# Optimization experiments

Hardware: AMD Instinct MI355X
Metric: run time of the kernel (lower is better)

Reference implementation:

```python
import jax, jax.numpy as jnp
import numpy as np

B, T, C, H = 4, 2048, 1024, 16
D = C // H  # head_dim = 64


def setup_inputs() -> dict:
    key = jax.random.key(0)
    ks = jax.random.split(key, 5)
    scale = 0.02
    return {
        "x": jax.random.normal(ks[0], (B, T, C), dtype=jnp.float32),
        "w_qkv": jax.random.normal(ks[1], (C, 3 * C), dtype=jnp.float32) * scale,
        "b_qkv": jnp.zeros((3 * C,), dtype=jnp.float32),
        "w_out": jax.random.normal(ks[2], (C, C), dtype=jnp.float32) * scale,
        "b_out": jnp.zeros((C,), dtype=jnp.float32),
    }


def reference(x, w_qkv, b_qkv, w_out, b_out):
    Bx, Tx, Cx = x.shape
    qkv = x @ w_qkv + b_qkv  # [B,T,3C]
    q, k, v = jnp.split(qkv, 3, axis=-1)
    # [B,T,C] -> [B,H,T,D]
    def heads(t):
        return t.reshape(Bx, Tx, H, D).transpose(0, 2, 1, 3)
    q, k, v = heads(q), heads(k), heads(v)
    scores = jnp.einsum("bhtd,bhsd->bhts", q, k) / jnp.sqrt(jnp.float32(D))
    causal = jnp.tril(jnp.ones((Tx, Tx), dtype=bool))
    scores = jnp.where(causal[None, None], scores, -jnp.inf)
    attn = jax.nn.softmax(scores, axis=-1)
    y = jnp.einsum("bhts,bhsd->bhtd", attn, v)  # [B,H,T,D]
    y = y.transpose(0, 2, 1, 3).reshape(Bx, Tx, Cx)
    return y @ w_out + b_out
```

## Files before the change

kernel.cpp:

```cpp
#include <hip/hip_runtime.h>
#include <hip/hip_bf16.h>
#include <math.h>

typedef __bf16 bf16;
typedef __bf16 bf16x8 __attribute__((ext_vector_type(8)));
typedef __bf16 bf16x4 __attribute__((ext_vector_type(4)));
typedef __bf16 bf16x2 __attribute__((ext_vector_type(2)));
typedef float  f32x4  __attribute__((ext_vector_type(4)));

__device__ __forceinline__ void gld_lds16(const bf16* g, bf16* l) {
    void* gv = (void*)g;
    __builtin_amdgcn_global_load_lds(
        (__attribute__((address_space(1))) void*)gv,
        (__attribute__((address_space(3))) void*)l, 16, 0, 0);
}

__global__ void k_cvt_bf16(const float* __restrict__ in, bf16* __restrict__ out, int n4) {
    int i = blockIdx.x * blockDim.x + threadIdx.x;
    if (i < n4) {
        float4 v = ((const float4*)in)[i];
        bf16x4 o;
        o[0] = (bf16)v.x; o[1] = (bf16)v.y; o[2] = (bf16)v.z; o[3] = (bf16)v.w;
        ((bf16x4*)out)[i] = o;
    }
}

__global__ void k_transpose_cvt(const float* __restrict__ in, bf16* __restrict__ out,
                                int R, int C) {
    __shared__ float tile[64][68];
    int c0 = blockIdx.x * 64, r0 = blockIdx.y * 64;
    int tid = threadIdx.x;
#pragma unroll
    for (int i = 0; i < 4; ++i) {
        int chunk = tid + i * 256;
        int r = chunk >> 4, c4 = (chunk & 15) * 4;
        float4 v = *(const float4*)(in + (size_t)(r0 + r) * C + c0 + c4);
        tile[r][c4 + 0] = v.x; tile[r][c4 + 1] = v.y;
        tile[r][c4 + 2] = v.z; tile[r][c4 + 3] = v.w;
    }
    __syncthreads();
#pragma unroll
    for (int i = 0; i < 2; ++i) {
        int chunk = tid + i * 256;
        int c = chunk >> 3, k8 = (chunk & 7) * 8;
        bf16x8 v;
#pragma unroll
        for (int j = 0; j < 8; ++j) v[j] = (bf16)tile[k8 + j][c];
        *(bf16x8*)(out + (size_t)(c0 + c) * R + r0 + k8) = v;
    }
}

__global__ void k_transpose_v(const bf16* __restrict__ qkv, bf16* __restrict__ vt) {
    __shared__ bf16 tile[64][72];
    int bh = blockIdx.y, b = bh >> 4, h = bh & 15;
    int t0 = blockIdx.x * 64;
    int tid = threadIdx.x;
    const bf16* src = qkv + (size_t)(b * 2048 + t0) * 3072 + 2048 + h * 64;
#pragma unroll
    for (int i = 0; i < 2; ++i) {
        int chunk = tid + i * 256;
        int t = chunk >> 3, d8 = (chunk & 7) * 8;
        bf16x8 v = *(const bf16x8*)(src + (size_t)t * 3072 + d8);
#pragma unroll
        for (int j = 0; j < 8; ++j) tile[t][d8 + j] = v[j];
    }
    __syncthreads();
#pragma unroll
    for (int i = 0; i < 2; ++i) {
        int chunk = tid + i * 256;
        int d = chunk >> 3, t8 = (chunk & 7) * 8;
        bf16x8 v;
#pragma unroll
        for (int j = 0; j < 8; ++j) v[j] = tile[t8 + j][d];
        *(bf16x8*)(vt + ((size_t)bh * 64 + d) * 2048 + t0 + t8) = v;
    }
}

template <bool OUT_BF16>
__global__ __launch_bounds__(256, 2) void k_gemm(
    const bf16* __restrict__ A, const bf16* __restrict__ Bt,
    const float* __restrict__ bias, void* __restrict__ Cout,
    int M, int N, int K) {
    __shared__ __align__(16) bf16 lA[2][4096];
    __shared__ __align__(16) bf16 lB[2][4096];
    int tid = threadIdx.x;
    int wid = tid >> 6, lane = tid & 63;
    int quad = lane >> 4, l16 = lane & 15;
    int bm = blockIdx.y * 128, bn = blockIdx.x * 128;
    int wm = (wid >> 1) * 64, wn = (wid & 1) * 64;

    f32x4 zero = {0.f, 0.f, 0.f, 0.f};
    f32x4 acc[4][4];
#pragma unroll
    for (int i = 0; i < 4; ++i)
#pragma unroll
        for (int j = 0; j < 4; ++j) acc[i][j] = zero;

    for (int k0 = 0; k0 < K; k0 += 64) {
        __syncthreads();
#pragma unroll
        for (int i = 0; i < 4; ++i) {
            int j = (wid * 4 + i) * 64 + lane;
            int kf = j >> 9, row = (j & 511) >> 2, c8 = (j & 3) * 8;
            gld_lds16(A  + (size_t)(bm + row) * K + k0 + kf * 32 + c8, &lA[0][0] + (wid * 4 + i) * 512);
            gld_lds16(Bt + (size_t)(bn + row) * K + k0 + kf * 32 + c8, &lB[0][0] + (wid * 4 + i) * 512);
        }
        __syncthreads();
#pragma unroll
        for (int kk = 0; kk < 2; ++kk) {
            bf16x8 af[4], bg[4];
#pragma unroll
            for (int i = 0; i < 4; ++i) {
                af[i] = *(const bf16x8*)(&lA[kk][(wm + i * 16 + l16) * 32 + quad * 8]);
                bg[i] = *(const bf16x8*)(&lB[kk][(wn + i * 16 + l16) * 32 + quad * 8]);
            }
#pragma unroll
            for (int i = 0; i < 4; ++i)
#pragma unroll
                for (int j = 0; j < 4; ++j)
                    acc[i][j] = __builtin_amdgcn_mfma_f32_16x16x32_bf16(af[i], bg[j], acc[i][j], 0, 0, 0);
        }
    }
#pragma unroll
    for (int i = 0; i < 4; ++i) {
#pragma unroll
        for (int j = 0; j < 4; ++j) {
            int col = bn + wn + j * 16 + l16;
            float bv = bias ? bias[col] : 0.f;
#pragma unroll
            for (int r = 0; r < 4; ++r) {
                int row = bm + wm + i * 16 + quad * 4 + r;
                float v = acc[i][j][r] + bv;
                if (OUT_BF16) ((bf16*)Cout)[(size_t)row * N + col] = (bf16)v;
                else          ((float*)Cout)[(size_t)row * N + col] = v;
            }
        }
    }
}

__global__ __launch_bounds__(256, 4) void k_attn(
    const bf16* __restrict__ qkv,
    const bf16* __restrict__ vt,
    bf16* __restrict__ y) {
    __shared__ __align__(16) bf16 lK[2][4096];
    __shared__ __align__(16) bf16 lV[2][4096];

    const int T = 2048, CQ = 3072;
    int tid = threadIdx.x, wid = tid >> 6, lane = tid & 63;
    int quad = lane >> 4, l16 = lane & 15;
    int lo = quad & 1, hi2 = quad >> 1;
    int x = blockIdx.x;
    int bh = ((x & 7) << 3) | ((x >> 3) & 7);
    int qb = 15 - (x >> 6);
    int b = bh >> 4, h = bh & 15;
    int q0 = qb * 128;
    int rb = qb * 4 + wid;
    int mdiag = rb >> 1;
    int ntiles = qb * 2 + 2;

    const bf16* qbase = qkv + (size_t)(b * T + q0 + wid * 32) * CQ + h * 64;
    const bf16* kbase = qkv + (size_t)(b * T) * CQ + 1024 + h * 64;
    const bf16* vbase = vt + (size_t)bh * 64 * T;

    auto stage = [&](int kt, int buf) {
        int t0 = kt * 64;
#pragma unroll
        for (int i = 0; i < 2; ++i) {
            int j = (wid * 2 + i) * 64 + lane;
            int r = j >> 3;
            int cs = ((j ^ r) & 7) * 8;
            gld_lds16(kbase + (size_t)(t0 + r) * CQ + cs, &lK[buf][(wid * 2 + i) * 512]);
            gld_lds16(vbase + (size_t)r * T + t0 + cs,    &lV[buf][(wid * 2 + i) * 512]);
        }
    };

    const float QSCALE = 0.125f * 1.44269504088896341f;
    bf16x8 qf[2][2];
#pragma unroll
    for (int qi = 0; qi < 2; ++qi)
#pragma unroll
        for (int kf = 0; kf < 2; ++kf) {
            bf16x8 v = *(const bf16x8*)(qbase + (size_t)(qi * 16 + l16) * CQ + kf * 32 + quad * 8);
#pragma unroll
            for (int j = 0; j < 8; ++j) v[j] = (bf16)((float)v[j] * QSCALE);
            qf[qi][kf] = v;
        }

    f32x4 zero = {0.f, 0.f, 0.f, 0.f};
    f32x4 minit = {-14.4269504089f, -14.4269504089f, -14.4269504089f, -14.4269504089f};
    f32x4 o[2][4];
    f32x4 ls[2];
#pragma unroll
    for (int qi = 0; qi < 2; ++qi) {
        ls[qi] = zero;
#pragma unroll
        for (int i = 0; i < 4; ++i) o[qi][i] = zero;
    }

    int bpA = (lo * 2 + hi2) * 64 + l16 * 4;
    int bpB = (lo * 2 + (hi2 ^ 1)) * 64 + l16 * 4;
    bf16x8 ones;
#pragma unroll
    for (int j = 0; j < 8; ++j) ones[j] = (bf16)1.0f;

    stage(0, 0);
    for (int kt = 0; kt < ntiles; ++kt) {
        __syncthreads();
        if (kt + 1 < ntiles) stage(kt + 1, (kt + 1) & 1);
        if (kt > mdiag) continue;
        const bf16* Kb = lK[kt & 1];
        const bf16* Vb = lV[kt & 1];
        bool diag = (kt == mdiag);
        bool half = diag && !(rb & 1);
        int in_hi = half ? 2 : 4;

        f32x4 s[2][4];
#pragma unroll
        for (int qi = 0; qi < 2; ++qi)
#pragma unroll
            for (int in = 0; in < 4; ++in) s[qi][in] = minit;
#pragma unroll
        for (int kf = 0; kf < 2; ++kf)
            for (int in = 0; in < in_hi; ++in) {
                bf16x8 kb = *(const bf16x8*)(Kb + (in * 16 + l16) * 64 + (((kf * 4 + quad) ^ (l16 & 7)) * 8));
#pragma unroll
                for (int qi = 0; qi < 2; ++qi)
                    s[qi][in] = __builtin_amdgcn_mfma_f32_16x16x32_bf16(kb, qf[qi][kf], s[qi][in], 0, 0, 0);
            }

        int rl0 = (rb * 32) - kt * 64;
        int pk[2][4][2];
#pragma unroll
        for (int qi = 0; qi < 2; ++qi) {
            int qloc = rl0 + qi * 16 + l16;
#pragma unroll
            for (int in = 0; in < 4; ++in) {
                if (in >= in_hi) { pk[qi][in][0] = 0; pk[qi][in][1] = 0; continue; }
                float e[4];
#pragma unroll
                for (int r = 0; r < 4; ++r) {
                    float ev = __builtin_amdgcn_exp2f(s[qi][in][r]);
                    if (diag) {
                        int tloc = in * 16 + quad * 4 + r;
                        if (tloc > qloc) ev = 0.f;
                    }
                    e[r] = ev;
                }
#pragma unroll
                for (int p = 0; p < 2; ++p) {
                    bf16x2 pr;
                    pr[0] = (bf16)e[2 * p];
                    pr[1] = (bf16)e[2 * p + 1];
                    pk[qi][in][p] = __builtin_bit_cast(int, pr);
                }
            }
        }

#pragma unroll
        for (int kf = 0; kf < 2; ++kf) {
            bf16x8 vb[4];
#pragma unroll
            for (int dn = 0; dn < 4; ++dn)
                vb[dn] = *(const bf16x8*)(Vb + (dn * 16 + l16) * 64 + (((kf * 4 + quad) ^ (l16 & 7)) * 8));
#pragma unroll
            for (int qi = 0; qi < 2; ++qi) {
                int v0 = lo ? pk[qi][kf * 2 + 1][0] : pk[qi][kf * 2][0];
                int v1 = lo ? pk[qi][kf * 2 + 1][1] : pk[qi][kf * 2][1];
                int v2 = lo ? pk[qi][kf * 2][0]     : pk[qi][kf * 2 + 1][0];
                int v3 = lo ? pk[qi][kf * 2][1]     : pk[qi][kf * 2 + 1][1];
                int r0 = __builtin_amdgcn_ds_bpermute(bpA, v0);
                int r1 = __builtin_amdgcn_ds_bpermute(bpA, v1);
                int r2 = __builtin_amdgcn_ds_bpermute(bpB, v2);
                int r3 = __builtin_amdgcn_ds_bpermute(bpB, v3);
                int4 wv;
                wv.x = hi2 ? r2 : r0;
                wv.y = hi2 ? r3 : r1;
                wv.z = hi2 ? r0 : r2;
                wv.w = hi2 ? r1 : r3;
                bf16x8 pa = __builtin_bit_cast(bf16x8, wv);
                ls[qi] = __builtin_amdgcn_mfma_f32_16x16x32_bf16(pa, ones, ls[qi], 0, 0, 0);
#pragma unroll
                for (int dn = 0; dn < 4; ++dn)
                    o[qi][dn] = __builtin_amdgcn_mfma_f32_16x16x32_bf16(pa, vb[dn], o[qi][dn], 0, 0, 0);
            }
        }
    }

#pragma unroll
    for (int qi = 0; qi < 2; ++qi)
#pragma unroll
        for (int r = 0; r < 4; ++r) {
            float li = 1.f / ls[qi][r];
            int row = q0 + wid * 32 + qi * 16 + quad * 4 + r;
#pragma unroll
            for (int dn = 0; dn < 4; ++dn) {
                float v = o[qi][dn][r] * li;
                y[(size_t)(b * T + row) * 1024 + h * 64 + dn * 16 + l16] = (bf16)v;
            }
        }
}

extern "C" void kernel_launch(void* const* d_in, const int* in_sizes, int n_in,
                              void* d_out, int out_size, void* d_ws, size_t ws_size,
                              hipStream_t stream) {
    const float* x     = (const float*)d_in[0];
    const float* w_qkv = (const float*)d_in[1];
    const float* b_qkv = (const float*)d_in[2];
    const float* w_out = (const float*)d_in[3];
    const float* b_out = (const float*)d_in[4];
    float* out = (float*)d_out;

    const int B = 4, T = 2048, C = 1024, H = 16;
    const int M = B * T;

    char* ws = (char*)d_ws;
    bf16* xb    = (bf16*)(ws);
    bf16* wqkvT = (bf16*)(ws + (16ull << 20));
    bf16* woutT = (bf16*)(ws + (22ull << 20));
    bf16* qkvb  = (bf16*)(ws + (24ull << 20));
    bf16* yb    = (bf16*)(ws + (72ull << 20));
    bf16* vtb   = xb;

    k_cvt_bf16<<<(M * C / 4 + 255) / 256, 256, 0, stream>>>(x, xb, M * C / 4);
    k_transpose_cvt<<<dim3(3 * C / 64, C / 64), 256, 0, stream>>>(w_qkv, wqkvT, C, 3 * C);
    k_transpose_cvt<<<dim3(C / 64, C / 64), 256, 0, stream>>>(w_out, woutT, C, C);
    k_gemm<true><<<dim3(3 * C / 128, M / 128), 256, 0, stream>>>(xb, wqkvT, b_qkv, qkvb, M, 3 * C, C);
    k_transpose_v<<<dim3(T / 64, B * H), 256, 0, stream>>>(qkvb, vtb);
    k_attn<<<dim3(1024, 1), 256, 0, stream>>>(qkvb, vtb, yb);
    k_gemm<false><<<dim3(C / 128, M / 128), 256, 0, stream>>>(yb, woutT, b_out, out, M, C, C);
}
```

Before: 289.5 us.

## Fuse V transpose into QKV GEMM epilogue and rebalance attention block order

Measured after the change: 307.7 us. 1.06x slower.

```diff
diff --git a/kernel.cpp b/kernel.cpp
--- a/kernel.cpp
+++ b/kernel.cpp
@@ -50,36 +50,11 @@
     }
 }
 
-__global__ void k_transpose_v(const bf16* __restrict__ qkv, bf16* __restrict__ vt) {
-    __shared__ bf16 tile[64][72];
-    int bh = blockIdx.y, b = bh >> 4, h = bh & 15;
-    int t0 = blockIdx.x * 64;
-    int tid = threadIdx.x;
-    const bf16* src = qkv + (size_t)(b * 2048 + t0) * 3072 + 2048 + h * 64;
-#pragma unroll
-    for (int i = 0; i < 2; ++i) {
-        int chunk = tid + i * 256;
-        int t = chunk >> 3, d8 = (chunk & 7) * 8;
-        bf16x8 v = *(const bf16x8*)(src + (size_t)t * 3072 + d8);
-#pragma unroll
-        for (int j = 0; j < 8; ++j) tile[t][d8 + j] = v[j];
-    }
-    __syncthreads();
-#pragma unroll
-    for (int i = 0; i < 2; ++i) {
-        int chunk = tid + i * 256;
-        int d = chunk >> 3, t8 = (chunk & 7) * 8;
-        bf16x8 v;
-#pragma unroll
-        for (int j = 0; j < 8; ++j) v[j] = tile[t8 + j][d];
-        *(bf16x8*)(vt + ((size_t)bh * 64 + d) * 2048 + t0 + t8) = v;
-    }
-}
-
-template <bool OUT_BF16>
+template <bool OUT_BF16, bool VSPLIT>
 __global__ __launch_bounds__(256, 2) void k_gemm(
     const bf16* __restrict__ A, const bf16* __restrict__ Bt,
     const float* __restrict__ bias, void* __restrict__ Cout,
+    bf16* __restrict__ vt,
     int M, int N, int K) {
     __shared__ __align__(16) bf16 lA[2][4096];
     __shared__ __align__(16) bf16 lB[2][4096];
@@ -121,6 +96,25 @@
                     acc[i][j] = __builtin_amdgcn_mfma_f32_16x16x32_bf16(af[i], bg[j], acc[i][j], 0, 0, 0);
         }
     }
+    if (VSPLIT && bn >= 2048) {
+#pragma unroll
+        for (int i = 0; i < 4; ++i) {
+#pragma unroll
+            for (int j = 0; j < 4; ++j) {
+                int col = bn + wn + j * 16 + l16;
+                float bv = bias ? bias[col] : 0.f;
+                int dd = col - 2048;
+                int row0 = bm + wm + i * 16 + quad * 4;
+                int bh = ((row0 >> 11) << 4) | (dd >> 6);
+                int d = dd & 63;
+                bf16x4 pv;
+#pragma unroll
+                for (int r = 0; r < 4; ++r) pv[r] = (bf16)(acc[i][j][r] + bv);
+                *(bf16x4*)(vt + ((size_t)(bh * 64 + d)) * 2048 + (row0 & 2047)) = pv;
+            }
+        }
+        return;
+    }
 #pragma unroll
     for (int i = 0; i < 4; ++i) {
 #pragma unroll
@@ -151,7 +145,9 @@
     int lo = quad & 1, hi2 = quad >> 1;
     int x = blockIdx.x;
     int bh = ((x & 7) << 3) | ((x >> 3) & 7);
-    int qb = 15 - (x >> 6);
+    int kk4 = x >> 8;
+    int tt4 = (x >> 6) & 3;
+    int qb = 4 * ((kk4 + tt4) & 3) + kk4;
     int b = bh >> 4, h = bh & 15;
     int q0 = qb * 128;
     int rb = qb * 4 + wid;
@@ -318,14 +314,15 @@
     bf16* wqkvT = (bf16*)(ws + (16ull << 20));
     bf16* woutT = (bf16*)(ws + (22ull << 20));
     bf16* qkvb  = (bf16*)(ws + (24ull << 20));
-    bf16* yb    = (bf16*)(ws + (72ull << 20));
-    bf16* vtb   = xb;
+    bf16* vtb   = (bf16*)(ws + (72ull << 20));
+    bf16* yb    = xb;
 
     k_cvt_bf16<<<(M * C / 4 + 255) / 256, 256, 0, stream>>>(x, xb, M * C / 4);
     k_transpose_cvt<<<dim3(3 * C / 64, C / 64), 256, 0, stream>>>(w_qkv, wqkvT, C, 3 * C);
     k_transpose_cvt<<<dim3(C / 64, C / 64), 256, 0, stream>>>(w_out, woutT, C, C);
-    k_gemm<true><<<dim3(3 * C / 128, M / 128), 256, 0, stream>>>(xb, wqkvT, b_qkv, qkvb, M, 3 * C, C);
-    k_transpose_v<<<dim3(T / 64, B * H), 256, 0, stream>>>(qkvb, vtb);
+    k_gemm<true, true><<<dim3(3 * C / 128, M / 128), 256, 0, stream>>>(
+        xb, wqkvT, b_qkv, qkvb, vtb, M, 3 * C, C);
     k_attn<<<dim3(1024, 1), 256, 0, stream>>>(qkvb, vtb, yb);
-    k_gemm<false><<<dim3(C / 128, M / 128), 256, 0, stream>>>(yb, woutT, b_out, out, M, C, C);
-}
+    k_gemm<false, false><<<dim3(C / 128, M / 128), 256, 0, stream>>>(
+        yb, woutT, b_out, out, nullptr, M, C, C);
+}
```
